# Kernel optimization log

Hardware: AMD Instinct MI355X
Metric: run time of the kernel (lower is better)

Reference implementation:

```python
import jax, jax.numpy as jnp
import numpy as np


def _reverse_sequence(x, lens):
    # TF-style reverse_sequence along axis 1: reverse the first lens[b] entries of row b.
    T = x.shape[1]
    t = jnp.arange(T)
    idx = jnp.where(t[None, :] < lens[:, None], lens[:, None] - 1 - t[None, :], t[None, :])
    idx = idx.reshape(idx.shape + (1,) * (x.ndim - 2))
    return jnp.take_along_axis(x, idx, axis=1)


def _crf_decode(potentials, transitions, seq_lens):
    # potentials: [B, T, O], transitions: [O, O], seq_lens: [B]
    B, T, O = potentials.shape
    init = potentials[:, 0, :]                                   # [B, O]
    valid = jnp.arange(1, T)[:, None] < seq_lens[None, :]        # [T-1, B]
    xs_pot = jnp.transpose(potentials[:, 1:, :], (1, 0, 2))      # [T-1, B, O]

    def fwd_step(state, xs):
        x_t, v = xs
        ts = state[:, :, None] + transitions[None, :, :]         # [B, prev, cur]
        new_state = jnp.where(v[:, None], x_t + jnp.max(ts, axis=1), state)
        bp = jnp.argmax(ts, axis=1).astype(jnp.int32)            # [B, O]
        sc = jnp.max(jax.nn.softmax(ts, axis=1), axis=1)         # [B, O] confidence of best transition
        return new_state, (bp, sc)

    last_score, (bps, scs) = jax.lax.scan(fwd_step, init, (xs_pot, valid))
    lens1 = jnp.maximum(seq_lens - 1, 0)
    bps = _reverse_sequence(jnp.transpose(bps, (1, 0, 2)), lens1)   # [B, T-1, O]
    scs = _reverse_sequence(jnp.transpose(scs, (1, 0, 2)), lens1)

    init_tag = jnp.argmax(last_score, axis=1).astype(jnp.int32)     # [B]
    init_conf = jnp.max(jax.nn.softmax(last_score, axis=1), axis=1) # [B]

    def bwd_step(tag, xs):
        bp_t, sc_t = xs
        new_tag = jnp.take_along_axis(bp_t, tag[:, None], axis=1)[:, 0]
        new_sc = jnp.take_along_axis(sc_t, tag[:, None], axis=1)[:, 0]
        return new_tag, (new_tag, new_sc)

    _, (tags, scores) = jax.lax.scan(
        bwd_step, init_tag,
        (jnp.transpose(bps, (1, 0, 2)), jnp.transpose(scs, (1, 0, 2))))
    decode_tags = _reverse_sequence(jnp.concatenate([init_tag[:, None], tags.T], axis=1), seq_lens)
    decode_scores = _reverse_sequence(jnp.concatenate([init_conf[:, None], scores.T], axis=1), seq_lens)
    return decode_tags, decode_scores


def setup_inputs() -> dict:
    key = jax.random.key(0)
    k1, k2, k3 = jax.random.split(key, 3)
    B, T, O = 512, 512, 64
    logits = jax.random.normal(k1, (B, T, O), dtype=jnp.float32)
    sequence_lengths = jax.random.randint(k2, (B,), 1, T + 1, dtype=jnp.int32)
    transition_params = jax.random.normal(k3, (O, O), dtype=jnp.float32) * 0.1
    return {"logits": logits, "transition_params": transition_params,
            "sequence_lengths": sequence_lengths}


def reference(logits, transition_params, sequence_lengths):
    pred_ids, scores = _crf_decode(logits, transition_params, sequence_lengths)
    T = pred_ids.shape[1]
    mask = jnp.arange(T)[None, :] < sequence_lengths[:, None]
    predicted_ids = pred_ids * mask.astype(pred_ids.dtype)
    confidence_values = scores * mask.astype(scores.dtype)
    return predicted_ids, confidence_values
```

## Files before the change

kernel.cpp:

```cpp
#include <hip/hip_runtime.h>
#include <math.h>

#define BB 512
#define TT 512
#define OO 64

typedef float f32x4 __attribute__((ext_vector_type(4)));

__global__ void crf_transpose(const float* __restrict__ trans,
                              float* __restrict__ Tt) {
    for (int k = threadIdx.x; k < OO * OO; k += 256)
        Tt[k] = trans[(k & 63) * OO + (k >> 6)];
}

__global__ __launch_bounds__(64, 1) void crf_scan(
    const float* __restrict__ logits,
    const float* __restrict__ trans,
    const int*   __restrict__ seqlens,
    float* __restrict__ out_tags,
    float* __restrict__ Mst)
{
    const int b = blockIdx.x;
    const int j = threadIdx.x;

    __shared__ __align__(16) float st[OO];
    __shared__ float Tt_lds[OO * OO];
    __shared__ unsigned char tagl[TT];

    const int L = seqlens[b];
    const float* lg = logits + (size_t)b * TT * OO;
    float* Mw = Mst + (size_t)b * TT * OO;

    {
        const f32x4* rowp = (const f32x4*)(trans + j * OO);
        #pragma unroll
        for (int q = 0; q < 16; ++q) {
            f32x4 rv = rowp[q];
            Tt_lds[(4*q+0) * OO + j] = rv[0];
            Tt_lds[(4*q+1) * OO + j] = rv[1];
            Tt_lds[(4*q+2) * OO + j] = rv[2];
            Tt_lds[(4*q+3) * OO + j] = rv[3];
        }
    }
    float Tc[64];
    #pragma unroll
    for (int r = 0; r < 64; ++r)
        Tc[r] = trans[r * OO + j];

    const unsigned stbase = (unsigned)(size_t)&st[0];
    const unsigned wrAddr = stbase + (unsigned)(j * 4);

    float s = lg[j];
    Mw[j] = 0.f;
    asm volatile("ds_write_b32 %0, %1" :: "v"(wrAddr), "v"(s));

    float xr1 = lg[1 * OO + j];
    float xr2 = lg[2 * OO + j];
    float xr3 = lg[3 * OO + j];
    float xr4 = lg[4 * OO + j];

    const float* lgp = lg + 5 * OO + j;
    float*       mwp = Mw + OO + j;

    for (int t = 1; t < L; ++t) {
        float x = xr1; xr1 = xr2; xr2 = xr3; xr3 = xr4;
        xr4 = *lgp;
        if (t < TT - 5) lgp += OO;

        f32x4 r0,r1,r2,r3,r4,r5,r6,r7,r8,r9,r10,r11,r12,r13,r14,r15;
        asm volatile(
            "ds_read_b128 %0, %16 offset:0\n\t"
            "ds_read_b128 %1, %16 offset:16\n\t"
            "ds_read_b128 %2, %16 offset:32\n\t"
            "ds_read_b128 %3, %16 offset:48\n\t"
            "ds_read_b128 %4, %16 offset:64\n\t"
            "ds_read_b128 %5, %16 offset:80\n\t"
            "ds_read_b128 %6, %16 offset:96\n\t"
            "ds_read_b128 %7, %16 offset:112\n\t"
            "ds_read_b128 %8, %16 offset:128\n\t"
            "ds_read_b128 %9, %16 offset:144\n\t"
            "ds_read_b128 %10, %16 offset:160\n\t"
            "ds_read_b128 %11, %16 offset:176\n\t"
            "ds_read_b128 %12, %16 offset:192\n\t"
            "ds_read_b128 %13, %16 offset:208\n\t"
            "ds_read_b128 %14, %16 offset:224\n\t"
            "ds_read_b128 %15, %16 offset:240\n\t"
            "s_waitcnt lgkmcnt(0)"
            : "=&v"(r0), "=&v"(r1), "=&v"(r2), "=&v"(r3),
              "=&v"(r4), "=&v"(r5), "=&v"(r6), "=&v"(r7),
              "=&v"(r8), "=&v"(r9), "=&v"(r10), "=&v"(r11),
              "=&v"(r12), "=&v"(r13), "=&v"(r14), "=&v"(r15)
            : "v"(stbase));
        __builtin_amdgcn_sched_barrier(0);

        float m0, m1, m2, m3;
        #define QUAD(q, rr, acc, first)                                   \
        {                                                                 \
            float c0 = rr[0] + Tc[4*(q)+0];                               \
            float c1 = rr[1] + Tc[4*(q)+1];                               \
            float c2 = rr[2] + Tc[4*(q)+2];                               \
            float c3 = rr[3] + Tc[4*(q)+3];                               \
            float mq = fmaxf(fmaxf(fmaxf(c0, c1), c2), c3);               \
            acc = first ? mq : fmaxf(acc, mq);                            \
        }
        QUAD(0,  r0,  m0, 1) QUAD(1,  r1,  m1, 1)
        QUAD(2,  r2,  m2, 1) QUAD(3,  r3,  m3, 1)
        QUAD(4,  r4,  m0, 0) QUAD(5,  r5,  m1, 0)
        QUAD(6,  r6,  m2, 0) QUAD(7,  r7,  m3, 0)
        QUAD(8,  r8,  m0, 0) QUAD(9,  r9,  m1, 0)
        QUAD(10, r10, m2, 0) QUAD(11, r11, m3, 0)
        QUAD(12, r12, m0, 0) QUAD(13, r13, m1, 0)
        QUAD(14, r14, m2, 0) QUAD(15, r15, m3, 0)
        #undef QUAD
        float m = fmaxf(fmaxf(m0, m1), fmaxf(m2, m3));

        *mwp = m; mwp += OO;
        s = x + m;
        asm volatile("ds_write_b32 %0, %1" :: "v"(wrAddr), "v"(s));
    }

    float mm = s;
    #pragma unroll
    for (int d = 1; d < 64; d <<= 1)
        mm = fmaxf(mm, __shfl_xor(mm, d));
    unsigned long long bal = __ballot(s == mm);
    int gcur = (int)__builtin_ctzll(bal);

    int t = L - 1;
    if (j == 0) tagl[t] = (unsigned char)gcur;

    float Mt = Mw[t * OO + j];
    float Xp = (t >= 1) ? lg[(t - 1) * OO + j] : 0.f;
    float Mp = (t >= 1) ? Mw[(t - 1) * OO + j] : 0.f;
    float Xq = (t >= 2) ? lg[(t - 2) * OO + j] : 0.f;
    float Mq = (t >= 2) ? Mw[(t - 2) * OO + j] : 0.f;

    while (t >= 1) {
        float target = __uint_as_float(
            (unsigned)__builtin_amdgcn_readlane(__float_as_uint(Mt), gcur));
        float d = (Xp + Mp) + Tt_lds[gcur * OO + j];
        unsigned long long bl = __ballot(d == target);
        gcur = (int)__builtin_ctzll(bl);
        if (j == 0) tagl[t - 1] = (unsigned char)gcur;
        Mt = Mp; Xp = Xq; Mp = Mq;
        if (t >= 3) {
            Xq = lg[(t - 3) * OO + j];
            Mq = Mw[(t - 3) * OO + j];
        }
        --t;
    }
    asm volatile("" ::: "memory");

    float* ot = out_tags + (size_t)b * TT;
    for (int p = j; p < TT; p += 64)
        ot[p] = (p < L) ? (float)tagl[p] : 0.f;
}

__global__ __launch_bounds__(256) void crf_conf(
    const float* __restrict__ logits,
    const float* __restrict__ Mst,
    const float* __restrict__ Tt,
    const float* __restrict__ out_tags,
    const int*   __restrict__ seqlens,
    float* __restrict__ out_scores)
{
    const int b = blockIdx.x >> 7;
    const int p = ((blockIdx.x & 127) << 2) + (threadIdx.x >> 6);
    const int i = threadIdx.x & 63;
    const int L = seqlens[b];

    if (p >= L) {
        if (i == 0) out_scores[(size_t)b * TT + p] = 0.f;
        return;
    }

    const size_t row = ((size_t)b * TT + p) * OO;
    float v = logits[row + i] + Mst[row + i];
    if (p < L - 1) {
        int g = (int)out_tags[(size_t)b * TT + p + 1];
        v += Tt[g * OO + i];
    }

    float m = v;
    #pragma unroll
    for (int d = 1; d < 64; d <<= 1)
        m = fmaxf(m, __shfl_xor(m, d));
    float e = __expf(v - m);
    #pragma unroll
    for (int d = 1; d < 64; d <<= 1)
        e += __shfl_xor(e, d);

    if (i == 0)
        out_scores[(size_t)b * TT + p] = 1.0f / e;
}

__global__ __launch_bounds__(256) void crf_decode_fallback(
    const float* __restrict__ logits,
    const float* __restrict__ trans,
    const int*   __restrict__ seqlens,
    float* __restrict__ out)
{
    const int b   = blockIdx.x;
    const int tid = threadIdx.x;
    const int j   = tid >> 2;
    const int c   = tid & 3;

    __shared__ unsigned char bpl[TT][OO];
    __shared__ unsigned char scl[TT][OO];
    __shared__ float st2[2][OO];

    const int L = seqlens[b];
    const float* lg = logits + (size_t)b * TT * OO;

    float trc[16];
    #pragma unroll
    for (int i2 = 0; i2 < 16; ++i2)
        trc[i2] = trans[(c * 16 + i2) * OO + j];

    if (tid < OO) st2[0][tid] = lg[tid];
    __syncthreads();

    int cur = 0;
    for (int t = 1; t < L; ++t) {
        float x = lg[t * OO + j];
        float v[16];
        float m = -1e30f;
        int   idx = 0;
        #pragma unroll
        for (int i2 = 0; i2 < 16; ++i2) {
            float val = st2[cur][c * 16 + i2] + trc[i2];
            v[i2] = val;
            if (val > m) { m = val; idx = c * 16 + i2; }
        }
        #pragma unroll
        for (int d = 1; d <= 2; d <<= 1) {
            float mo = __shfl_xor(m, d);
            int   io = __shfl_xor(idx, d);
            if (mo > m || (mo == m && io < idx)) { m = mo; idx = io; }
        }
        float sden = 0.f;
        #pragma unroll
        for (int i2 = 0; i2 < 16; ++i2)
            sden += __expf(v[i2] - m);
        #pragma unroll
        for (int d = 1; d <= 2; d <<= 1)
            sden += __shfl_xor(sden, d);

        if (c == 0) {
            st2[cur ^ 1][j] = x + m;
            bpl[t][j] = (unsigned char)idx;
            float conf = fminf(1.0f / sden, 1.0f);
            scl[t][j] = (unsigned char)(conf * 255.0f + 0.5f);
        }
        cur ^= 1;
        __syncthreads();
    }

    if (tid == 0) {
        float m = -1e30f; int idx = 0;
        for (int jj = 0; jj < OO; ++jj) {
            float vv = st2[cur][jj];
            if (vv > m) { m = vv; idx = jj; }
        }
        float sden = 0.f;
        for (int jj = 0; jj < OO; ++jj)
            sden += __expf(st2[cur][jj] - m);

        float* out_tags   = out + (size_t)b * TT;
        float* out_scores = out + (size_t)BB * TT + (size_t)b * TT;
        out_tags[L - 1]   = (float)idx;
        out_scores[L - 1] = 1.0f / sden;

        int tag = idx;
        for (int t = L - 1; t >= 1; --t) {
            int ntag  = bpl[t][tag];
            float sc  = (float)scl[t][tag] * (1.0f / 255.0f);
            out_tags[t - 1]   = (float)ntag;
            out_scores[t - 1] = sc;
            tag = ntag;
        }
    }

    float* out_tags   = out + (size_t)b * TT;
    float* out_scores = out + (size_t)BB * TT + (size_t)b * TT;
    for (int p = L + tid; p < TT; p += 256) {
        out_tags[p]   = 0.f;
        out_scores[p] = 0.f;
    }
}

extern "C" void kernel_launch(void* const* d_in, const int* in_sizes, int n_in,
                              void* d_out, int out_size, void* d_ws, size_t ws_size,
                              hipStream_t stream) {
    const float* logits = (const float*)d_in[0];
    const float* trans  = (const float*)d_in[1];
    const int*   lens   = (const int*)d_in[2];
    float* out = (float*)d_out;

    const size_t m_bytes  = (size_t)BB * TT * OO * sizeof(float);
    const size_t tt_bytes = (size_t)OO * OO * sizeof(float);
    if (ws_size >= m_bytes + tt_bytes) {
        float* Mst = (float*)d_ws;
        float* Tt  = (float*)((char*)d_ws + m_bytes);
        float* out_tags   = out;
        float* out_scores = out + (size_t)BB * TT;

        crf_transpose<<<1, 256, 0, stream>>>(trans, Tt);
        crf_scan<<<BB, 64, 0, stream>>>(logits, trans, lens, out_tags, Mst);
        crf_conf<<<BB * 128, 256, 0, stream>>>(logits, Mst, Tt, out_tags, lens,
                                               out_scores);
    } else {
        crf_decode_fallback<<<BB, 256, 0, stream>>>(logits, trans, lens, out);
    }
}
```

Measured before the change: 377.2 us.

## Stage logits into LDS ring buffer via async global_load_lds in forward scan

Replaces the per-step register-rotated global loads of logits with a double-buffered 16-row LDS ring filled 8 rows at a time by global_load_lds, and fuses the state write, state reads and next logit read into one DS batch issued before the next iteration's wait. The loop now runs a fixed TT iterations with predicated state updates rather than stopping at L, and stores the max values through inline assembly. The aim is to take global-load latency off the serial dependency chain and overlap LDS traffic with compute. In exchange, sequences shorter than TT now do wasted iterations, and correctness depends on hand-placed vmcnt and lgkmcnt waits.

```diff
diff --git a/kernel.cpp b/kernel.cpp
--- a/kernel.cpp
+++ b/kernel.cpp
@@ -11,6 +11,15 @@
                               float* __restrict__ Tt) {
     for (int k = threadIdx.x; k < OO * OO; k += 256)
         Tt[k] = trans[(k & 63) * OO + (k >> 6)];
+}
+
+__device__ __forceinline__ void stage8(const float* gsrc_lane, float* ldst) {
+    __builtin_amdgcn_global_load_lds(
+        (const __attribute__((address_space(1))) unsigned int*)(gsrc_lane),
+        (__attribute__((address_space(3))) unsigned int*)(ldst), 16, 0, 0);
+    __builtin_amdgcn_global_load_lds(
+        (const __attribute__((address_space(1))) unsigned int*)(gsrc_lane + 256),
+        (__attribute__((address_space(3))) unsigned int*)(ldst + 256), 16, 0, 0);
 }
 
 __global__ __launch_bounds__(64, 1) void crf_scan(
@@ -24,6 +33,7 @@
     const int j = threadIdx.x;
 
     __shared__ __align__(16) float st[OO];
+    __shared__ __align__(16) float xl[16][OO];
     __shared__ float Tt_lds[OO * OO];
     __shared__ unsigned char tagl[TT];
 
@@ -42,67 +52,104 @@
             Tt_lds[(4*q+3) * OO + j] = rv[3];
         }
     }
+
     float Tc[64];
-    #pragma unroll
-    for (int r = 0; r < 64; ++r)
-        Tc[r] = trans[r * OO + j];
+    #define TCBLK(K)                                                      \
+    {                                                                     \
+        const float* bp = trans + (K) * 16 * OO + j;                      \
+        asm volatile(                                                     \
+            "global_load_dword %0, %16, off offset:0\n\t"                 \
+            "global_load_dword %1, %16, off offset:256\n\t"               \
+            "global_load_dword %2, %16, off offset:512\n\t"               \
+            "global_load_dword %3, %16, off offset:768\n\t"               \
+            "global_load_dword %4, %16, off offset:1024\n\t"              \
+            "global_load_dword %5, %16, off offset:1280\n\t"              \
+            "global_load_dword %6, %16, off offset:1536\n\t"              \
+            "global_load_dword %7, %16, off offset:1792\n\t"              \
+            "global_load_dword %8, %16, off offset:2048\n\t"              \
+            "global_load_dword %9, %16, off offset:2304\n\t"              \
+            "global_load_dword %10, %16, off offset:2560\n\t"             \
+            "global_load_dword %11, %16, off offset:2816\n\t"             \
+            "global_load_dword %12, %16, off offset:3072\n\t"             \
+            "global_load_dword %13, %16, off offset:3328\n\t"             \
+            "global_load_dword %14, %16, off offset:3584\n\t"             \
+            "global_load_dword %15, %16, off offset:3840\n\t"             \
+            "s_waitcnt vmcnt(0)"                                          \
+            : "=&v"(Tc[(K)*16+0]),  "=&v"(Tc[(K)*16+1]),                  \
+              "=&v"(Tc[(K)*16+2]),  "=&v"(Tc[(K)*16+3]),                  \
+              "=&v"(Tc[(K)*16+4]),  "=&v"(Tc[(K)*16+5]),                  \
+              "=&v"(Tc[(K)*16+6]),  "=&v"(Tc[(K)*16+7]),                  \
+              "=&v"(Tc[(K)*16+8]),  "=&v"(Tc[(K)*16+9]),                  \
+              "=&v"(Tc[(K)*16+10]), "=&v"(Tc[(K)*16+11]),                 \
+              "=&v"(Tc[(K)*16+12]), "=&v"(Tc[(K)*16+13]),                 \
+              "=&v"(Tc[(K)*16+14]), "=&v"(Tc[(K)*16+15])                  \
+            : "v"(bp));                                                   \
+    }
+    TCBLK(0) TCBLK(1) TCBLK(2) TCBLK(3)
+    #undef TCBLK
 
     const unsigned stbase = (unsigned)(size_t)&st[0];
     const unsigned wrAddr = stbase + (unsigned)(j * 4);
+    const unsigned xbase4 = (unsigned)(size_t)&xl[0][0] + (unsigned)(j * 4);
 
     float s = lg[j];
     Mw[j] = 0.f;
-    asm volatile("ds_write_b32 %0, %1" :: "v"(wrAddr), "v"(s));
-
-    float xr1 = lg[1 * OO + j];
-    float xr2 = lg[2 * OO + j];
-    float xr3 = lg[3 * OO + j];
-    float xr4 = lg[4 * OO + j];
-
-    const float* lgp = lg + 5 * OO + j;
-    float*       mwp = Mw + OO + j;
-
-    for (int t = 1; t < L; ++t) {
-        float x = xr1; xr1 = xr2; xr2 = xr3; xr3 = xr4;
-        xr4 = *lgp;
-        if (t < TT - 5) lgp += OO;
-
-        f32x4 r0,r1,r2,r3,r4,r5,r6,r7,r8,r9,r10,r11,r12,r13,r14,r15;
-        asm volatile(
-            "ds_read_b128 %0, %16 offset:0\n\t"
-            "ds_read_b128 %1, %16 offset:16\n\t"
-            "ds_read_b128 %2, %16 offset:32\n\t"
-            "ds_read_b128 %3, %16 offset:48\n\t"
-            "ds_read_b128 %4, %16 offset:64\n\t"
-            "ds_read_b128 %5, %16 offset:80\n\t"
-            "ds_read_b128 %6, %16 offset:96\n\t"
-            "ds_read_b128 %7, %16 offset:112\n\t"
-            "ds_read_b128 %8, %16 offset:128\n\t"
-            "ds_read_b128 %9, %16 offset:144\n\t"
-            "ds_read_b128 %10, %16 offset:160\n\t"
-            "ds_read_b128 %11, %16 offset:176\n\t"
-            "ds_read_b128 %12, %16 offset:192\n\t"
-            "ds_read_b128 %13, %16 offset:208\n\t"
-            "ds_read_b128 %14, %16 offset:224\n\t"
-            "ds_read_b128 %15, %16 offset:240\n\t"
-            "s_waitcnt lgkmcnt(0)"
-            : "=&v"(r0), "=&v"(r1), "=&v"(r2), "=&v"(r3),
-              "=&v"(r4), "=&v"(r5), "=&v"(r6), "=&v"(r7),
-              "=&v"(r8), "=&v"(r9), "=&v"(r10), "=&v"(r11),
-              "=&v"(r12), "=&v"(r13), "=&v"(r14), "=&v"(r15)
-            : "v"(stbase));
+
+    stage8(lg + j * 4, &xl[0][0]);
+    stage8(lg + 8 * OO + j * 4, &xl[8][0]);
+    asm volatile("s_waitcnt vmcnt(0)" ::: "memory");
+    __builtin_amdgcn_sched_barrier(0);
+
+    f32x4 r0,r1,r2,r3,r4,r5,r6,r7,r8,r9,r10,r11,r12,r13,r14,r15;
+    float xreg;
+
+    #define DSBATCH(XADDR)                                                \
+        asm volatile(                                                     \
+            "ds_write_b32 %18, %19\n\t"                                   \
+            "ds_read_b128 %0, %17 offset:0\n\t"                           \
+            "ds_read_b128 %1, %17 offset:16\n\t"                          \
+            "ds_read_b128 %2, %17 offset:32\n\t"                          \
+            "ds_read_b128 %3, %17 offset:48\n\t"                          \
+            "ds_read_b128 %4, %17 offset:64\n\t"                          \
+            "ds_read_b128 %5, %17 offset:80\n\t"                          \
+            "ds_read_b128 %6, %17 offset:96\n\t"                          \
+            "ds_read_b128 %7, %17 offset:112\n\t"                         \
+            "ds_read_b128 %8, %17 offset:128\n\t"                         \
+            "ds_read_b128 %9, %17 offset:144\n\t"                         \
+            "ds_read_b128 %10, %17 offset:160\n\t"                        \
+            "ds_read_b128 %11, %17 offset:176\n\t"                        \
+            "ds_read_b128 %12, %17 offset:192\n\t"                        \
+            "ds_read_b128 %13, %17 offset:208\n\t"                        \
+            "ds_read_b128 %14, %17 offset:224\n\t"                        \
+            "ds_read_b128 %15, %17 offset:240\n\t"                        \
+            "ds_read_b32 %16, %20\n\t"                                    \
+            : "=&v"(r0), "=&v"(r1), "=&v"(r2), "=&v"(r3),                 \
+              "=&v"(r4), "=&v"(r5), "=&v"(r6), "=&v"(r7),                 \
+              "=&v"(r8), "=&v"(r9), "=&v"(r10), "=&v"(r11),               \
+              "=&v"(r12), "=&v"(r13), "=&v"(r14), "=&v"(r15), "=&v"(xreg) \
+            : "v"(stbase), "v"(wrAddr), "v"(s), "v"(XADDR))
+
+    #define QUAD(q, rr, acc, first)                                       \
+    {                                                                     \
+        float c0 = rr[0] + Tc[4*(q)+0];                                   \
+        float c1 = rr[1] + Tc[4*(q)+1];                                   \
+        float c2 = rr[2] + Tc[4*(q)+2];                                   \
+        float c3 = rr[3] + Tc[4*(q)+3];                                   \
+        float mq = fmaxf(fmaxf(fmaxf(c0, c1), c2), c3);                   \
+        acc = first ? mq : fmaxf(acc, mq);                                \
+    }
+
+    DSBATCH(xbase4 + 256u);
+
+    float* mwp = Mw + OO + j;
+    const float* stgp = lg + 16 * OO + j * 4;
+
+    for (int t = 1; t < TT; ++t) {
+        asm volatile("s_waitcnt lgkmcnt(0)");
         __builtin_amdgcn_sched_barrier(0);
+        float x = xreg;
 
         float m0, m1, m2, m3;
-        #define QUAD(q, rr, acc, first)                                   \
-        {                                                                 \
-            float c0 = rr[0] + Tc[4*(q)+0];                               \
-            float c1 = rr[1] + Tc[4*(q)+1];                               \
-            float c2 = rr[2] + Tc[4*(q)+2];                               \
-            float c3 = rr[3] + Tc[4*(q)+3];                               \
-            float mq = fmaxf(fmaxf(fmaxf(c0, c1), c2), c3);               \
-            acc = first ? mq : fmaxf(acc, mq);                            \
-        }
         QUAD(0,  r0,  m0, 1) QUAD(1,  r1,  m1, 1)
         QUAD(2,  r2,  m2, 1) QUAD(3,  r3,  m3, 1)
         QUAD(4,  r4,  m0, 0) QUAD(5,  r5,  m1, 0)
@@ -111,13 +158,34 @@
         QUAD(10, r10, m2, 0) QUAD(11, r11, m3, 0)
         QUAD(12, r12, m0, 0) QUAD(13, r13, m1, 0)
         QUAD(14, r14, m2, 0) QUAD(15, r15, m3, 0)
-        #undef QUAD
         float m = fmaxf(fmaxf(m0, m1), fmaxf(m2, m3));
 
-        *mwp = m; mwp += OO;
-        s = x + m;
-        asm volatile("ds_write_b32 %0, %1" :: "v"(wrAddr), "v"(s));
-    }
+        if ((t & 7) == 7) {
+            int c = (t >> 3) + 2;
+            if (c < 64) {
+                __builtin_amdgcn_sched_barrier(0);
+                stage8(stgp, &xl[(c & 1) * 8][0]);
+                __builtin_amdgcn_sched_barrier(0);
+                stgp += 8 * OO;
+            }
+        }
+
+        asm volatile("global_store_dword %0, %1, off" :: "v"(mwp), "v"(m));
+        mwp += OO;
+        s = (t < L) ? (x + m) : s;
+
+        if ((t & 7) == 7) {
+            asm volatile("s_waitcnt vmcnt(9)" ::: "memory");
+            __builtin_amdgcn_sched_barrier(0);
+        }
+        unsigned xaddr = xbase4 + (((unsigned)((t + 1) & 15)) << 8);
+        DSBATCH(xaddr);
+    }
+    #undef QUAD
+    #undef DSBATCH
+
+    asm volatile("s_waitcnt vmcnt(0) lgkmcnt(0)" ::: "memory");
+    __builtin_amdgcn_sched_barrier(0);
 
     float mm = s;
     #pragma unroll
```

After: 386.4 us. +2.4%, slower.
